# Kernel tuning notes

Hardware: AMD Instinct MI355X
Metric: run time of the kernel (lower is better)

The kernel has to match this reference:

```python
import jax, jax.numpy as jnp
import numpy as np

TOP_K = 8
NUM_EXPERTS = 64
N_TOKENS = 16384
N_EMBED = 4096
EPS = 1e-12  # F.normalize default eps


def setup_inputs() -> dict:
    key = jax.random.key(0)
    k_x, k_wr, k_br, k_wn, k_bn, k_noise = jax.random.split(key, 6)
    scale = 1.0 / np.sqrt(N_EMBED)
    return {
        "x": jax.random.normal(k_x, (N_TOKENS, N_EMBED), dtype=jnp.float32),
        "w_route": jax.random.normal(k_wr, (N_EMBED, NUM_EXPERTS), dtype=jnp.float32) * scale,
        "b_route": jax.random.normal(k_br, (NUM_EXPERTS,), dtype=jnp.float32) * scale,
        "w_noise": jax.random.normal(k_wn, (N_EMBED, NUM_EXPERTS), dtype=jnp.float32) * scale,
        "b_noise": jax.random.normal(k_bn, (NUM_EXPERTS,), dtype=jnp.float32) * scale,
        "noise": jax.random.normal(k_noise, (N_TOKENS, NUM_EXPERTS), dtype=jnp.float32),
    }


def _l1_normalize(v):
    return v / jnp.maximum(jnp.sum(jnp.abs(v)), EPS)


def reference(x, w_route, b_route, w_noise, b_noise, noise):
    # dual linear projections: [N, D] @ [D, E] -> [N, E]
    logits = x @ w_route + b_route
    noise_logits = x @ w_noise + b_noise
    noisy_logits = logits + noise * jax.nn.softplus(noise_logits)

    # top-k (sorted descending, matches torch.topk)
    top_vals, top_idx = jax.lax.top_k(noisy_logits, TOP_K)  # [N, K]
    rows = jnp.arange(noisy_logits.shape[0])[:, None]

    # scatter top-k logits into -inf, softmax -> sparse gate distribution
    sparse_logits = jnp.full_like(noisy_logits, -jnp.inf).at[rows, top_idx].set(top_vals)
    router_output = jax.nn.softmax(sparse_logits, axis=-1)  # [N, E]

    # aux loss (training path). Faithful to torch scatter semantics:
    # gates[n, top_idx[n, j]] = router_output[n, j] (first K columns of src).
    probs = jax.nn.softmax(noisy_logits, axis=-1)
    gates = jnp.zeros_like(probs).at[rows, top_idx].set(router_output[:, :TOP_K])
    probs_sum = probs.sum(0)                                  # [E]
    freq = (gates > 0).astype(jnp.float32).sum(0)             # [E]
    lsesq = jnp.sum(jax.nn.logsumexp(noisy_logits, axis=-1) ** 2)
    switchloss = NUM_EXPERTS * jnp.sum(_l1_normalize(probs_sum) * _l1_normalize(freq))
    zloss = lsesq / noisy_logits.shape[0]
    aux_loss = switchloss + 0.1 * zloss

    return router_output, top_idx, aux_loss
```

## Files before the change

### kernel.cpp

```cpp
#include <hip/hip_runtime.h>
#include <math.h>

#define NT 16384
#define NE 4096
#define NX 64
#define TK 8

#define BM 32
#define NBLK (NT / BM)
#define NSTEP 64

#define RO_SIZE (NT * NX)
#define TI_OFF  RO_SIZE
#define AUX_IDX (RO_SIZE + NT * TK)

#define MAXFLAG 8192
#define PSB_IDX 8256
#define FRB_IDX (PSB_IDX + NBLK * 64)
#define L2B_IDX (FRB_IDX + NBLK * 64)
#define WS_FLOATS (L2B_IDX + NBLK)
#define BPACK_OFF (((WS_FLOATS * 4) + 255) & ~255)
#define BPACK_USHORTS (128 * 4 * 2 * 128 * 8)
#define WS_NEED ((size_t)BPACK_OFF + (size_t)BPACK_USHORTS * 2)

#define DELTA_FP32 5e-5f
#define DELTA_BF16 2.5e-4f

typedef __attribute__((ext_vector_type(8))) short bf16x8_t;
typedef __attribute__((ext_vector_type(4))) float f32x4_t;
typedef __attribute__((ext_vector_type(16))) float f32x16_t;

__device__ __forceinline__ float neginf() { return __int_as_float(0xff800000); }

__device__ __forceinline__ unsigned short bf16_trunc(float f) {
    return (unsigned short)(__float_as_uint(f) >> 16);
}
__device__ __forceinline__ unsigned short bf16_rtn(float f) {
    unsigned u = __float_as_uint(f);
    unsigned r = u + 0x7fffu + ((u >> 16) & 1u);
    return (unsigned short)(r >> 16);
}
__device__ __forceinline__ float bf16_to_f(unsigned short h) {
    return __uint_as_float(((unsigned)h) << 16);
}

__device__ __forceinline__ void split4(const float4& f,
                                       unsigned& h0, unsigned& h1,
                                       unsigned& l0, unsigned& l1) {
    unsigned u0 = __float_as_uint(f.x), u1 = __float_as_uint(f.y);
    unsigned u2 = __float_as_uint(f.z), u3 = __float_as_uint(f.w);
    h0 = __builtin_amdgcn_perm(u1, u0, 0x07060302u);
    h1 = __builtin_amdgcn_perm(u3, u2, 0x07060302u);
    float g0 = f.x - __uint_as_float(u0 & 0xffff0000u);
    float g1 = f.y - __uint_as_float(u1 & 0xffff0000u);
    float g2 = f.z - __uint_as_float(u2 & 0xffff0000u);
    float g3 = f.w - __uint_as_float(u3 & 0xffff0000u);
    l0 = __builtin_amdgcn_perm(__float_as_uint(g1), __float_as_uint(g0), 0x07060302u);
    l1 = __builtin_amdgcn_perm(__float_as_uint(g3), __float_as_uint(g2), 0x07060302u);
}

#define GLOAD16(GP, LP) __builtin_amdgcn_global_load_lds(                     \
    (const __attribute__((address_space(1))) void*)(GP),                      \
    (__attribute__((address_space(3))) void*)(LP), 16, 0, 0)

__global__ __launch_bounds__(512) void prep_w_kernel(
    const float* __restrict__ w_route, const float* __restrict__ w_noise,
    unsigned short* __restrict__ bp)
{
    const int kt = blockIdx.x;
    const int t = threadIdx.x;
    const int col = t & 127;
    const int kq = t >> 7;
    const float* src = (col < NX) ? (w_route + col) : (w_noise + (col - NX));
    const int kbase = kt * 32 + kq * 8;
    bf16x8_t h8, l8;
    #pragma unroll
    for (int i = 0; i < 8; ++i) {
        float v = src[(size_t)(kbase + i) * NX];
        unsigned short hh = bf16_trunc(v);
        h8[i] = (short)hh;
        l8[i] = (short)bf16_rtn(v - bf16_to_f(hh));
    }
    unsigned short* base = bp + ((size_t)((kt * 4 + kq) * 2) * 128 + col) * 8;
    *(bf16x8_t*)base = h8;
    *(bf16x8_t*)(base + 128 * 8) = l8;
}

__global__ __launch_bounds__(512, 4) void fused32_kernel(
    const float* __restrict__ x,
    const unsigned short* __restrict__ bp,
    const float* __restrict__ b_route, const float* __restrict__ b_noise,
    const float* __restrict__ noise,
    float* __restrict__ out,
    float* __restrict__ ps_blk, float* __restrict__ fr_blk,
    float* __restrict__ lse2_blk,
    int* __restrict__ flag_cnt, int* __restrict__ flag_list)
{
    __shared__ __align__(16) char ldsraw[81920];

    const int tid = threadIdx.x;
    const int wid = tid >> 6;
    const int lane = tid & 63;
    const int l31 = lane & 31;
    const int lhi = lane >> 5;
    const int cgq = wid & 3;
    const int kh = wid >> 2;
    const int bm = blockIdx.x * BM;

    const int srow = tid >> 4;
    const int sq = tid & 15;
    const int skc = sq >> 1;
    const int shalf = sq & 1;
    const int srl = srow & 15;
    const int offA = srow * 256 + ((skc ^ srl) << 4) + shalf * 8;
    const float* sxa = x + (size_t)(bm + srow) * NE + sq * 4;

    char* ldsB = ldsraw + 16384;
    char* dB = ldsB + tid * 16;

    #define STAGE_B(BUF, ST) do {                                             \
        const unsigned short* sB_ = bp + (size_t)(ST) * 16384 + tid * 8;      \
        char* dB_ = dB + (BUF) * 32768;                                       \
        GLOAD16(sB_,         dB_);                                            \
        GLOAD16(sB_ + 4096,  dB_ + 8192);                                     \
        GLOAD16(sB_ + 8192,  dB_ + 16384);                                    \
        GLOAD16(sB_ + 12288, dB_ + 24576);                                    \
    } while (0)

    #define WRITE_A(BUF, RX) do {                                             \
        unsigned h0_, h1_, l0_, l1_;                                          \
        split4(RX, h0_, h1_, l0_, l1_);                                       \
        const int ob_ = (BUF) * 8192;                                         \
        *(int2*)(ldsraw + ob_ + offA)         = make_int2((int)h0_, (int)h1_);\
        *(int2*)(ldsraw + ob_ + (offA ^ 128)) = make_int2((int)l0_, (int)l1_);\
    } while (0)

    f32x16_t acc;
    #pragma unroll
    for (int i = 0; i < 16; ++i) acc[i] = 0.f;

    const int r15 = l31 & 15;
    const int adrA0 = l31 * 256 + (((4 * kh + 0 + lhi) ^ r15) << 4);
    const int adrA1 = l31 * 256 + (((4 * kh + 2 + lhi) ^ r15) << 4);
    const int offB = kh * 16384 + lhi * 4096 + (cgq * 32 + l31) * 16;

    #define COMPUTE(CUR) do {                                                 \
        const char* aB_ = ldsraw + (CUR) * 8192;                              \
        const char* bT_ = ldsB + (CUR) * 32768;                               \
        bf16x8_t ah0 = *(const bf16x8_t*)(aB_ + adrA0);                       \
        bf16x8_t al0 = *(const bf16x8_t*)(aB_ + (adrA0 ^ 128));               \
        bf16x8_t bh0 = *(const bf16x8_t*)(bT_ + offB);                        \
        bf16x8_t bl0 = *(const bf16x8_t*)(bT_ + offB + 2048);                 \
        acc = __builtin_amdgcn_mfma_f32_32x32x16_bf16(ah0, bh0, acc, 0, 0, 0);\
        acc = __builtin_amdgcn_mfma_f32_32x32x16_bf16(al0, bh0, acc, 0, 0, 0);\
        acc = __builtin_amdgcn_mfma_f32_32x32x16_bf16(ah0, bl0, acc, 0, 0, 0);\
        bf16x8_t ah1 = *(const bf16x8_t*)(aB_ + adrA1);                       \
        bf16x8_t al1 = *(const bf16x8_t*)(aB_ + (adrA1 ^ 128));               \
        bf16x8_t bh1 = *(const bf16x8_t*)(bT_ + offB + 8192);                 \
        bf16x8_t bl1 = *(const bf16x8_t*)(bT_ + offB + 8192 + 2048);          \
        acc = __builtin_amdgcn_mfma_f32_32x32x16_bf16(ah1, bh1, acc, 0, 0, 0);\
        acc = __builtin_amdgcn_mfma_f32_32x32x16_bf16(al1, bh1, acc, 0, 0, 0);\
        acc = __builtin_amdgcn_mfma_f32_32x32x16_bf16(ah1, bl1, acc, 0, 0, 0);\
    } while (0)

    float4 rxA = *(const float4*)(sxa);
    STAGE_B(0, 0);
    WRITE_A(0, rxA);
    float4 rxB = *(const float4*)(sxa + 64);
    __syncthreads();

    for (int t = 0; t < NSTEP; t += 2) {
        if (t + 2 < NSTEP) rxA = *(const float4*)(sxa + (t + 2) * 64);
        if (t + 1 < NSTEP) STAGE_B(1, t + 1);
        COMPUTE(0);
        if (t + 1 < NSTEP) WRITE_A(1, rxB);
        __syncthreads();
        if (t + 3 < NSTEP) rxB = *(const float4*)(sxa + (t + 3) * 64);
        if (t + 2 < NSTEP) STAGE_B(0, t + 2);
        COMPUTE(1);
        if (t + 2 < NSTEP) WRITE_A(0, rxA);
        __syncthreads();
    }
    #undef STAGE_B
    #undef WRITE_A
    #undef COMPUTE

    float (*part)[32][132] = (float (*)[32][132])ldsraw;
    #pragma unroll
    for (int r = 0; r < 16; ++r) {
        int row = (r & 3) + 8 * (r >> 2) + 4 * lhi;
        part[kh][row][cgq * 32 + l31] = acc[r];
    }
    __syncthreads();

    const float br = b_route[lane];
    const float bnv = b_noise[lane];
    float ps_l = 0.f, fr_l = 0.f, l2_l = 0.f;

    for (int tt = 0; tt < 4; ++tt) {
        const int tok = wid * 4 + tt;
        const int gt  = bm + tok;
        float lr = part[0][tok][lane] + part[1][tok][lane] + br;
        float ln = part[0][tok][64 + lane] + part[1][tok][64 + lane] + bnv;
        float nz = noise[(size_t)gt * NX + lane];
        float sp = fmaxf(ln, 0.f) + log1pf(expf(-fabsf(ln)));
        float v  = lr + nz * sp;

        float vv = v;
        float tv[9]; int ti[9];
        #pragma unroll
        for (int s = 0; s < 9; ++s) {
            float mv = vv; int mi = lane;
            #pragma unroll
            for (int off = 32; off > 0; off >>= 1) {
                float ov = __shfl_xor(mv, off);
                int   oi = __shfl_xor(mi, off);
                if (ov > mv || (ov == mv && oi < mi)) { mv = ov; mi = oi; }
            }
            tv[s] = mv; ti[s] = mi;
            if (lane == mi) vv = neginf();
        }

        float ming = 1e30f;
        #pragma unroll
        for (int s = 0; s < 8; ++s) ming = fminf(ming, tv[s] - tv[s + 1]);
        if (lane == 0 && ming < DELTA_BF16) {
            int p = atomicAdd(flag_cnt, 1);
            if (p < MAXFLAG) flag_list[p] = gt;
        }

        const float m0 = tv[0];
        float e8[8], s8 = 0.f;
        #pragma unroll
        for (int s = 0; s < 8; ++s) { e8[s] = expf(tv[s] - m0); s8 += e8[s]; }
        float r = 0.f;
        #pragma unroll
        for (int s = 0; s < 8; ++s) if (ti[s] == lane) r = e8[s] / s8;
        out[(size_t)gt * NX + lane] = r;
        if (lane < TK) out[TI_OFF + (size_t)gt * TK + lane] = (float)ti[lane];

        float p = expf(v - m0);
        float s64 = p;
        #pragma unroll
        for (int off = 32; off > 0; off >>= 1) s64 += __shfl_xor(s64, off);
        ps_l += p / s64;
        if (lane == 0) { float lse = m0 + logf(s64); l2_l += lse * lse; }

        unsigned tm8 = 0;
        #pragma unroll
        for (int s = 0; s < 8; ++s) if (ti[s] < TK) tm8 |= (1u << ti[s]);
        #pragma unroll
        for (int s = 0; s < 8; ++s)
            if (ti[s] == lane && ((tm8 >> s) & 1u)) fr_l += 1.f;
    }

    float* sps = (float*)(ldsraw + 34816);
    float* sfr = (float*)(ldsraw + 34816 + 2048);
    float* sl2 = (float*)(ldsraw + 34816 + 4096);
    sps[wid * 64 + lane] = ps_l;
    sfr[wid * 64 + lane] = fr_l;
    if (lane == 0) sl2[wid] = l2_l;
    __syncthreads();
    if (wid == 0) {
        float a = 0.f, b = 0.f;
        #pragma unroll
        for (int w = 0; w < 8; ++w) {
            a += sps[w * 64 + lane];
            b += sfr[w * 64 + lane];
        }
        ps_blk[(size_t)blockIdx.x * 64 + lane] = a;
        fr_blk[(size_t)blockIdx.x * 64 + lane] = b;
        if (lane == 0) {
            float z = 0.f;
            #pragma unroll
            for (int w = 0; w < 8; ++w) z += sl2[w];
            lse2_blk[blockIdx.x] = z;
        }
    }
}

#define FBM 64
#define FBN 128
#define FBK 32
#define XPITCH (FBM + 4)
__global__ __launch_bounds__(256) void fused_router_kernel(
    const float* __restrict__ x,
    const float* __restrict__ w_route, const float* __restrict__ b_route,
    const float* __restrict__ w_noise, const float* __restrict__ b_noise,
    const float* __restrict__ noise,
    float* __restrict__ out,
    float* __restrict__ ps_acc, float* __restrict__ fr_acc,
    float* __restrict__ lse2_acc,
    int* __restrict__ flag_cnt, int* __restrict__ flag_list)
{
    __shared__ float smem[FBM * FBN];
    float* xs  = smem;
    float* wst = smem + FBK * XPITCH;
    const int tid = threadIdx.x;
    const int block_m = blockIdx.x * FBM;
    const int row0 = (tid >> 5) * 8;
    const int col0 = (tid & 31) * 4;
    float acc[8][4];
    #pragma unroll
    for (int i = 0; i < 8; ++i)
        #pragma unroll
        for (int j = 0; j < 4; ++j) acc[i][j] = 0.f;
    float4 px[2], pw[4];
    {
        #pragma unroll
        for (int s = 0; s < 2; ++s) {
            int f = tid + s * 256, r = f >> 3, kqv = f & 7;
            px[s] = *reinterpret_cast<const float4*>(x + (size_t)(block_m + r) * NE + kqv * 4);
        }
        #pragma unroll
        for (int s = 0; s < 4; ++s) {
            int f = tid + s * 256, kk = f >> 5, c4 = (f & 31) * 4;
            const float* src = (c4 < NX) ? (w_route + (size_t)kk * NX + c4)
                                         : (w_noise + (size_t)kk * NX + (c4 - NX));
            pw[s] = *reinterpret_cast<const float4*>(src);
        }
    }
    for (int t = 0; t < NE / FBK; ++t) {
        __syncthreads();
        #pragma unroll
        for (int s = 0; s < 2; ++s) {
            int f = tid + s * 256, r = f >> 3, kqv = f & 7;
            xs[(kqv * 4 + 0) * XPITCH + r] = px[s].x;
            xs[(kqv * 4 + 1) * XPITCH + r] = px[s].y;
            xs[(kqv * 4 + 2) * XPITCH + r] = px[s].z;
            xs[(kqv * 4 + 3) * XPITCH + r] = px[s].w;
        }
        #pragma unroll
        for (int s = 0; s < 4; ++s) {
            int f = tid + s * 256, kk = f >> 5, c4 = (f & 31) * 4;
            *reinterpret_cast<float4*>(&wst[kk * FBN + c4]) = pw[s];
        }
        __syncthreads();
        if (t + 1 < NE / FBK) {
            const int k0 = (t + 1) * FBK;
            #pragma unroll
            for (int s = 0; s < 2; ++s) {
                int f = tid + s * 256, r = f >> 3, kqv = f & 7;
                px[s] = *reinterpret_cast<const float4*>(x + (size_t)(block_m + r) * NE + k0 + kqv * 4);
            }
            #pragma unroll
            for (int s = 0; s < 4; ++s) {
                int f = tid + s * 256, kk = f >> 5, c4 = (f & 31) * 4;
                const float* src = (c4 < NX) ? (w_route + (size_t)(k0 + kk) * NX + c4)
                                             : (w_noise + (size_t)(k0 + kk) * NX + (c4 - NX));
                pw[s] = *reinterpret_cast<const float4*>(src);
            }
        }
        #pragma unroll
        for (int k = 0; k < FBK; ++k) {
            float4 xa = *reinterpret_cast<const float4*>(&xs[k * XPITCH + row0]);
            float4 xb = *reinterpret_cast<const float4*>(&xs[k * XPITCH + row0 + 4]);
            float4 wv = *reinterpret_cast<const float4*>(&wst[k * FBN + col0]);
            float xf[8] = {xa.x, xa.y, xa.z, xa.w, xb.x, xb.y, xb.z, xb.w};
            float wf[4] = {wv.x, wv.y, wv.z, wv.w};
            #pragma unroll
            for (int i = 0; i < 8; ++i)
                #pragma unroll
                for (int j = 0; j < 4; ++j)
                    acc[i][j] = fmaf(xf[i], wf[j], acc[i][j]);
        }
    }
    __syncthreads();
    #pragma unroll
    for (int i = 0; i < 8; ++i) {
        float4 v = make_float4(acc[i][0], acc[i][1], acc[i][2], acc[i][3]);
        *reinterpret_cast<float4*>(&smem[(row0 + i) * FBN + col0]) = v;
    }
    __syncthreads();
    const int wave = tid >> 6;
    const int lane = tid & 63;
    const float br = b_route[lane];
    const float bnv = b_noise[lane];
    float ps_l = 0.f, fr_l = 0.f, l2_l = 0.f;
    for (int tt = 0; tt < FBM / 4; ++tt) {
        const int tok = wave * (FBM / 4) + tt;
        const int gt  = block_m + tok;
        float lr = smem[tok * FBN + lane] + br;
        float ln = smem[tok * FBN + NX + lane] + bnv;
        float nz = noise[(size_t)gt * NX + lane];
        float sp = fmaxf(ln, 0.f) + log1pf(expf(-fabsf(ln)));
        float v  = lr + nz * sp;
        float vv = v;
        float tv[9]; int ti[9];
        #pragma unroll
        for (int s = 0; s < 9; ++s) {
            float mv = vv; int mi = lane;
            #pragma unroll
            for (int off = 32; off > 0; off >>= 1) {
                float ov = __shfl_xor(mv, off);
                int   oi = __shfl_xor(mi, off);
                if (ov > mv || (ov == mv && oi < mi)) { mv = ov; mi = oi; }
            }
            tv[s] = mv; ti[s] = mi;
            if (lane == mi) vv = neginf();
        }
        float ming = 1e30f;
        #pragma unroll
        for (int s = 0; s < 8; ++s) ming = fminf(ming, tv[s] - tv[s + 1]);
        if (lane == 0 && ming < DELTA_FP32) {
            int p = atomicAdd(flag_cnt, 1);
            if (p < MAXFLAG) flag_list[p] = gt;
        }
        const float m0 = tv[0];
        float e8[8], s8 = 0.f;
        #pragma unroll
        for (int s = 0; s < 8; ++s) { e8[s] = expf(tv[s] - m0); s8 += e8[s]; }
        float r = 0.f;
        #pragma unroll
        for (int s = 0; s < 8; ++s) if (ti[s] == lane) r = e8[s] / s8;
        out[(size_t)gt * NX + lane] = r;
        if (lane < TK) out[TI_OFF + (size_t)gt * TK + lane] = (float)ti[lane];
        float p = expf(v - m0);
        float s64 = p;
        #pragma unroll
        for (int off = 32; off > 0; off >>= 1) s64 += __shfl_xor(s64, off);
        ps_l += p / s64;
        if (lane == 0) { float lse = m0 + logf(s64); l2_l += lse * lse; }
        unsigned tm8 = 0;
        #pragma unroll
        for (int s = 0; s < 8; ++s) if (ti[s] < TK) tm8 |= (1u << ti[s]);
        #pragma unroll
        for (int s = 0; s < 8; ++s)
            if (ti[s] == lane && ((tm8 >> s) & 1u)) fr_l += 1.f;
    }
    atomicAdd(&ps_acc[lane], ps_l);
    atomicAdd(&fr_acc[lane], fr_l);
    if (lane == 0) atomicAdd(lse2_acc, l2_l);
}

__global__ __launch_bounds__(256) void refine_kernel(
    const float* __restrict__ x, const float* __restrict__ w_route,
    const float* __restrict__ b_route, const float* __restrict__ w_noise,
    const float* __restrict__ b_noise, const float* __restrict__ noise,
    float* __restrict__ out, const int* __restrict__ flag_cnt,
    const int* __restrict__ flag_list)
{
    __shared__ double red[8][64];
    const int tid = threadIdx.x;
    const int lane = tid & 63, wq = tid >> 6;
    int nf = *flag_cnt; if (nf > MAXFLAG) nf = MAXFLAG;
    for (int fi = blockIdx.x; fi < nf; fi += gridDim.x) {
        const int gt = flag_list[fi];
        const float* xr = x + (size_t)gt * NE + wq * 1024;
        const float* wr = w_route + (size_t)wq * 1024 * NX;
        const float* wn = w_noise + (size_t)wq * 1024 * NX;
        double ar0 = 0, ar1 = 0, an0 = 0, an1 = 0;
        for (int k = 0; k < 1024; k += 2) {
            double x0 = xr[k], x1 = xr[k + 1];
            ar0 += x0 * (double)wr[(size_t)k * NX + lane];
            ar1 += x1 * (double)wr[(size_t)(k + 1) * NX + lane];
            an0 += x0 * (double)wn[(size_t)k * NX + lane];
            an1 += x1 * (double)wn[(size_t)(k + 1) * NX + lane];
        }
        red[wq * 2][lane]     = ar0 + ar1;
        red[wq * 2 + 1][lane] = an0 + an1;
        __syncthreads();
        if (tid < 64) {
            double lr = red[0][lane] + red[2][lane] + red[4][lane] + red[6][lane]
                      + (double)b_route[lane];
            double ln = red[1][lane] + red[3][lane] + red[5][lane] + red[7][lane]
                      + (double)b_noise[lane];
            double nz = (double)noise[(size_t)gt * NX + lane];
            double sp = (ln > 0.0) ? (ln + log1p(exp(-ln))) : log1p(exp(ln));
            double v  = lr + nz * sp;
            double vv = v;
            double tv[8]; int ti[8];
            #pragma unroll
            for (int s = 0; s < 8; ++s) {
                double mv = vv; int mi = lane;
                #pragma unroll
                for (int off = 32; off > 0; off >>= 1) {
                    double ov = __shfl_xor(mv, off);
                    int    oi = __shfl_xor(mi, off);
                    if (ov > mv || (ov == mv && oi < mi)) { mv = ov; mi = oi; }
                }
                tv[s] = mv; ti[s] = mi;
                if (lane == mi) vv = -1.0e300;
            }
            double m0 = tv[0], s8 = 0.0, e8[8];
            #pragma unroll
            for (int s = 0; s < 8; ++s) { e8[s] = exp(tv[s] - m0); s8 += e8[s]; }
            float r = 0.f;
            #pragma unroll
            for (int s = 0; s < 8; ++s) if (ti[s] == lane) r = (float)(e8[s] / s8);
            out[(size_t)gt * NX + lane] = r;
            if (lane < TK) out[TI_OFF + (size_t)gt * TK + lane] = (float)ti[lane];
        }
        __syncthreads();
    }
}

__global__ __launch_bounds__(512) void finalize_kernel(
    const float* __restrict__ ps_blk, const float* __restrict__ fr_blk,
    const float* __restrict__ lse2_blk, float* __restrict__ out)
{
    __shared__ float sps[8][64], sfr[8][64], sl2[512];
    const int t = threadIdx.x;
    const int e = t & 63, g = t >> 6;
    float a = 0.f, b = 0.f;
    for (int blk = g; blk < NBLK; blk += 8) {
        a += ps_blk[(size_t)blk * 64 + e];
        b += fr_blk[(size_t)blk * 64 + e];
    }
    sps[g][e] = a;
    sfr[g][e] = b;
    sl2[t] = lse2_blk[t];
    __syncthreads();
    if (t < 64) {
        float p = 0.f, f = 0.f;
        #pragma unroll
        for (int gg = 0; gg < 8; ++gg) { p += sps[gg][t]; f += sfr[gg][t]; }
        float z = 0.f;
        #pragma unroll
        for (int i = 0; i < 8; ++i) z += sl2[t * 8 + i];
        float sp = p, sf = f, sz = z;
        #pragma unroll
        for (int off = 32; off > 0; off >>= 1) {
            sp += __shfl_xor(sp, off);
            sf += __shfl_xor(sf, off);
            sz += __shfl_xor(sz, off);
        }
        float d = (p / fmaxf(sp, 1e-12f)) * (f / fmaxf(sf, 1e-12f));
        #pragma unroll
        for (int off = 32; off > 0; off >>= 1) d += __shfl_xor(d, off);
        if (t == 0)
            out[AUX_IDX] = 64.f * d + 0.1f * (sz / (float)NT);
    }
}

extern "C" void kernel_launch(void* const* d_in, const int* in_sizes, int n_in,
                              void* d_out, int out_size, void* d_ws, size_t ws_size,
                              hipStream_t stream) {
    const float* x       = (const float*)d_in[0];
    const float* w_route = (const float*)d_in[1];
    const float* b_route = (const float*)d_in[2];
    const float* w_noise = (const float*)d_in[3];
    const float* b_noise = (const float*)d_in[4];
    const float* noise   = (const float*)d_in[5];
    float* out = (float*)d_out;

    float* wsf = (float*)d_ws;
    int* flag_cnt  = (int*)wsf;
    int* flag_list = (int*)(wsf + 1);
    float* ps_blk   = wsf + PSB_IDX;
    float* fr_blk   = wsf + FRB_IDX;
    float* lse2_blk = wsf + L2B_IDX;

    hipMemsetAsync(d_ws, 0, (size_t)(1 + MAXFLAG) * sizeof(int), stream);

    if (ws_size >= WS_NEED) {
        unsigned short* bpack = (unsigned short*)((char*)d_ws + BPACK_OFF);
        prep_w_kernel<<<128, 512, 0, stream>>>(w_route, w_noise, bpack);
        fused32_kernel<<<NBLK, 512, 0, stream>>>(
            x, bpack, b_route, b_noise, noise, out,
            ps_blk, fr_blk, lse2_blk, flag_cnt, flag_list);
    } else {
        hipMemsetAsync(ps_blk, 0,
                       (size_t)(WS_FLOATS - PSB_IDX) * sizeof(float), stream);
        fused_router_kernel<<<NT / FBM, 256, 0, stream>>>(
            x, w_route, b_route, w_noise, b_noise, noise, out,
            ps_blk, fr_blk, lse2_blk, flag_cnt, flag_list);
    }

    refine_kernel<<<1024, 256, 0, stream>>>(
        x, w_route, b_route, w_noise, b_noise, noise, out, flag_cnt, flag_list);

    finalize_kernel<<<1, 512, 0, stream>>>(ps_blk, fr_blk, lse2_blk, out);
}
```

Baseline: 193.8 us.

## Split K four ways across waves, each wave computing two column tiles

Remaps the eight waves so that each covers a quarter of the K slice per step and computes two 32-column output tiles, instead of half of K for one tile. Each A fragment loaded from LDS now feeds two MFMA chains, which halves A reads per MFMA and gives two independent accumulator chains to hide MFMA latency. The cost is a second accumulator (more VGPRs), a four-way partial-sum reduction in LDS, and moving the reduction scratch to a higher LDS offset. A change to the fallback kernel's w_route pointer computes the same address as before.

```diff
diff --git a/kernel.cpp b/kernel.cpp
--- a/kernel.cpp
+++ b/kernel.cpp
@@ -103,8 +103,8 @@
     const int lane = tid & 63;
     const int l31 = lane & 31;
     const int lhi = lane >> 5;
-    const int cgq = wid & 3;
-    const int kh = wid >> 2;
+    const int cgp = wid & 1;
+    const int kh = wid >> 1;
     const int bm = blockIdx.x * BM;
 
     const int srow = tid >> 4;
@@ -135,32 +135,31 @@
         *(int2*)(ldsraw + ob_ + (offA ^ 128)) = make_int2((int)l0_, (int)l1_);\
     } while (0)
 
-    f32x16_t acc;
+    f32x16_t acc0, acc1;
     #pragma unroll
-    for (int i = 0; i < 16; ++i) acc[i] = 0.f;
+    for (int i = 0; i < 16; ++i) { acc0[i] = 0.f; acc1[i] = 0.f; }
 
     const int r15 = l31 & 15;
-    const int adrA0 = l31 * 256 + (((4 * kh + 0 + lhi) ^ r15) << 4);
-    const int adrA1 = l31 * 256 + (((4 * kh + 2 + lhi) ^ r15) << 4);
-    const int offB = kh * 16384 + lhi * 4096 + (cgq * 32 + l31) * 16;
+    const int adrA = l31 * 256 + (((2 * kh + lhi) ^ r15) << 4);
+    const int offB0 = (kh >> 1) * 16384 + ((kh & 1) * 2 + lhi) * 4096
+                    + (cgp * 64 + l31) * 16;
+    const int offB1 = offB0 + 512;
 
     #define COMPUTE(CUR) do {                                                 \
         const char* aB_ = ldsraw + (CUR) * 8192;                              \
         const char* bT_ = ldsB + (CUR) * 32768;                               \
-        bf16x8_t ah0 = *(const bf16x8_t*)(aB_ + adrA0);                       \
-        bf16x8_t al0 = *(const bf16x8_t*)(aB_ + (adrA0 ^ 128));               \
-        bf16x8_t bh0 = *(const bf16x8_t*)(bT_ + offB);                        \
-        bf16x8_t bl0 = *(const bf16x8_t*)(bT_ + offB + 2048);                 \
-        acc = __builtin_amdgcn_mfma_f32_32x32x16_bf16(ah0, bh0, acc, 0, 0, 0);\
-        acc = __builtin_amdgcn_mfma_f32_32x32x16_bf16(al0, bh0, acc, 0, 0, 0);\
-        acc = __builtin_amdgcn_mfma_f32_32x32x16_bf16(ah0, bl0, acc, 0, 0, 0);\
-        bf16x8_t ah1 = *(const bf16x8_t*)(aB_ + adrA1);                       \
-        bf16x8_t al1 = *(const bf16x8_t*)(aB_ + (adrA1 ^ 128));               \
-        bf16x8_t bh1 = *(const bf16x8_t*)(bT_ + offB + 8192);                 \
-        bf16x8_t bl1 = *(const bf16x8_t*)(bT_ + offB + 8192 + 2048);          \
-        acc = __builtin_amdgcn_mfma_f32_32x32x16_bf16(ah1, bh1, acc, 0, 0, 0);\
-        acc = __builtin_amdgcn_mfma_f32_32x32x16_bf16(al1, bh1, acc, 0, 0, 0);\
-        acc = __builtin_amdgcn_mfma_f32_32x32x16_bf16(ah1, bl1, acc, 0, 0, 0);\
+        bf16x8_t ah  = *(const bf16x8_t*)(aB_ + adrA);                        \
+        bf16x8_t al  = *(const bf16x8_t*)(aB_ + (adrA ^ 128));                \
+        bf16x8_t bh0 = *(const bf16x8_t*)(bT_ + offB0);                       \
+        bf16x8_t bh1 = *(const bf16x8_t*)(bT_ + offB1);                       \
+        bf16x8_t bl0 = *(const bf16x8_t*)(bT_ + offB0 + 2048);                \
+        bf16x8_t bl1 = *(const bf16x8_t*)(bT_ + offB1 + 2048);                \
+        acc0 = __builtin_amdgcn_mfma_f32_32x32x16_bf16(ah, bh0, acc0, 0, 0, 0);\
+        acc1 = __builtin_amdgcn_mfma_f32_32x32x16_bf16(ah, bh1, acc1, 0, 0, 0);\
+        acc0 = __builtin_amdgcn_mfma_f32_32x32x16_bf16(al, bh0, acc0, 0, 0, 0);\
+        acc1 = __builtin_amdgcn_mfma_f32_32x32x16_bf16(al, bh1, acc1, 0, 0, 0);\
+        acc0 = __builtin_amdgcn_mfma_f32_32x32x16_bf16(ah, bl0, acc0, 0, 0, 0);\
+        acc1 = __builtin_amdgcn_mfma_f32_32x32x16_bf16(ah, bl1, acc1, 0, 0, 0);\
     } while (0)
 
     float4 rxA = *(const float4*)(sxa);
@@ -189,7 +188,8 @@
     #pragma unroll
     for (int r = 0; r < 16; ++r) {
         int row = (r & 3) + 8 * (r >> 2) + 4 * lhi;
-        part[kh][row][cgq * 32 + l31] = acc[r];
+        part[kh][row][cgp * 64 + l31]      = acc0[r];
+        part[kh][row][cgp * 64 + 32 + l31] = acc1[r];
     }
     __syncthreads();
 
@@ -200,8 +200,10 @@
     for (int tt = 0; tt < 4; ++tt) {
         const int tok = wid * 4 + tt;
         const int gt  = bm + tok;
-        float lr = part[0][tok][lane] + part[1][tok][lane] + br;
-        float ln = part[0][tok][64 + lane] + part[1][tok][64 + lane] + bnv;
+        float lr = part[0][tok][lane] + part[1][tok][lane]
+                 + part[2][tok][lane] + part[3][tok][lane] + br;
+        float ln = part[0][tok][64 + lane] + part[1][tok][64 + lane]
+                 + part[2][tok][64 + lane] + part[3][tok][64 + lane] + bnv;
         float nz = noise[(size_t)gt * NX + lane];
         float sp = fmaxf(ln, 0.f) + log1pf(expf(-fabsf(ln)));
         float v  = lr + nz * sp;
@@ -254,9 +256,9 @@
             if (ti[s] == lane && ((tm8 >> s) & 1u)) fr_l += 1.f;
     }
 
-    float* sps = (float*)(ldsraw + 34816);
-    float* sfr = (float*)(ldsraw + 34816 + 2048);
-    float* sl2 = (float*)(ldsraw + 34816 + 4096);
+    float* sps = (float*)(ldsraw + 69632);
+    float* sfr = (float*)(ldsraw + 69632 + 2048);
+    float* sl2 = (float*)(ldsraw + 69632 + 4096);
     sps[wid * 64 + lane] = ps_l;
     sfr[wid * 64 + lane] = fr_l;
     if (lane == 0) sl2[wid] = l2_l;
@@ -346,8 +348,9 @@
             #pragma unroll
             for (int s = 0; s < 4; ++s) {
                 int f = tid + s * 256, kk = f >> 5, c4 = (f & 31) * 4;
-                const float* src = (c4 < NX) ? (w_route + (size_t)(k0 + kk) * NX + c4)
+                const float* src = (c4 < NX) ? (w_route + (size_t)kk * NX + c4)
                                              : (w_noise + (size_t)(k0 + kk) * NX + (c4 - NX));
+                if (c4 < NX) src = w_route + (size_t)(k0 + kk) * NX + c4;
                 pw[s] = *reinterpret_cast<const float4*>(src);
             }
         }
```

After: 199.9 us. 3.1% more time.

## Double block to 1024 threads with four-way K split in fused router kernel

Applied to the files above, without the earlier changes.

Launches the fused 32-token kernel with 1024 threads, so 16 waves split the K dimension four ways instead of two. Each wave now issues three MFMAs per stage instead of six, and each thread stages half as much of the packed weight tile. Only the first 512 threads load and split the x tile. The epilogue sums four partial accumulators and each wave handles two tokens instead of four. The aim is more in-flight waves to hide memory latency, at the cost of a larger LDS partial-sum region, extra reduction adds, and barriers over more waves.

```diff
diff --git a/kernel.cpp b/kernel.cpp
--- a/kernel.cpp
+++ b/kernel.cpp
@@ -86,7 +86,7 @@
     *(bf16x8_t*)(base + 128 * 8) = l8;
 }
 
-__global__ __launch_bounds__(512, 4) void fused32_kernel(
+__global__ __launch_bounds__(1024, 8) void fused32_kernel(
     const float* __restrict__ x,
     const unsigned short* __restrict__ bp,
     const float* __restrict__ b_route, const float* __restrict__ b_noise,
@@ -106,8 +106,9 @@
     const int cgq = wid & 3;
     const int kh = wid >> 2;
     const int bm = blockIdx.x * BM;
-
-    const int srow = tid >> 4;
+    const bool stager = (tid < 512);
+
+    const int srow = (tid >> 4) & 31;
     const int sq = tid & 15;
     const int skc = sq >> 1;
     const int shalf = sq & 1;
@@ -122,17 +123,17 @@
         const unsigned short* sB_ = bp + (size_t)(ST) * 16384 + tid * 8;      \
         char* dB_ = dB + (BUF) * 32768;                                       \
         GLOAD16(sB_,         dB_);                                            \
-        GLOAD16(sB_ + 4096,  dB_ + 8192);                                     \
         GLOAD16(sB_ + 8192,  dB_ + 16384);                                    \
-        GLOAD16(sB_ + 12288, dB_ + 24576);                                    \
     } while (0)
 
     #define WRITE_A(BUF, RX) do {                                             \
-        unsigned h0_, h1_, l0_, l1_;                                          \
-        split4(RX, h0_, h1_, l0_, l1_);                                       \
-        const int ob_ = (BUF) * 8192;                                         \
-        *(int2*)(ldsraw + ob_ + offA)         = make_int2((int)h0_, (int)h1_);\
-        *(int2*)(ldsraw + ob_ + (offA ^ 128)) = make_int2((int)l0_, (int)l1_);\
+        if (stager) {                                                         \
+            unsigned h0_, h1_, l0_, l1_;                                      \
+            split4(RX, h0_, h1_, l0_, l1_);                                   \
+            const int ob_ = (BUF) * 8192;                                     \
+            *(int2*)(ldsraw + ob_ + offA)         = make_int2((int)h0_, (int)h1_);\
+            *(int2*)(ldsraw + ob_ + (offA ^ 128)) = make_int2((int)l0_, (int)l1_);\
+        }                                                                     \
     } while (0)
 
     f32x16_t acc;
@@ -140,42 +141,36 @@
     for (int i = 0; i < 16; ++i) acc[i] = 0.f;
 
     const int r15 = l31 & 15;
-    const int adrA0 = l31 * 256 + (((4 * kh + 0 + lhi) ^ r15) << 4);
-    const int adrA1 = l31 * 256 + (((4 * kh + 2 + lhi) ^ r15) << 4);
-    const int offB = kh * 16384 + lhi * 4096 + (cgq * 32 + l31) * 16;
+    const int adrA = l31 * 256 + (((2 * kh + lhi) ^ r15) << 4);
+    const int offB = (kh >> 1) * 16384 + ((kh & 1) * 2 + lhi) * 4096
+                   + (cgq * 32 + l31) * 16;
 
     #define COMPUTE(CUR) do {                                                 \
         const char* aB_ = ldsraw + (CUR) * 8192;                              \
         const char* bT_ = ldsB + (CUR) * 32768;                               \
-        bf16x8_t ah0 = *(const bf16x8_t*)(aB_ + adrA0);                       \
-        bf16x8_t al0 = *(const bf16x8_t*)(aB_ + (adrA0 ^ 128));               \
-        bf16x8_t bh0 = *(const bf16x8_t*)(bT_ + offB);                        \
-        bf16x8_t bl0 = *(const bf16x8_t*)(bT_ + offB + 2048);                 \
-        acc = __builtin_amdgcn_mfma_f32_32x32x16_bf16(ah0, bh0, acc, 0, 0, 0);\
-        acc = __builtin_amdgcn_mfma_f32_32x32x16_bf16(al0, bh0, acc, 0, 0, 0);\
-        acc = __builtin_amdgcn_mfma_f32_32x32x16_bf16(ah0, bl0, acc, 0, 0, 0);\
-        bf16x8_t ah1 = *(const bf16x8_t*)(aB_ + adrA1);                       \
-        bf16x8_t al1 = *(const bf16x8_t*)(aB_ + (adrA1 ^ 128));               \
-        bf16x8_t bh1 = *(const bf16x8_t*)(bT_ + offB + 8192);                 \
-        bf16x8_t bl1 = *(const bf16x8_t*)(bT_ + offB + 8192 + 2048);          \
-        acc = __builtin_amdgcn_mfma_f32_32x32x16_bf16(ah1, bh1, acc, 0, 0, 0);\
-        acc = __builtin_amdgcn_mfma_f32_32x32x16_bf16(al1, bh1, acc, 0, 0, 0);\
-        acc = __builtin_amdgcn_mfma_f32_32x32x16_bf16(ah1, bl1, acc, 0, 0, 0);\
+        bf16x8_t ah = *(const bf16x8_t*)(aB_ + adrA);                         \
+        bf16x8_t al = *(const bf16x8_t*)(aB_ + (adrA ^ 128));                 \
+        bf16x8_t bh = *(const bf16x8_t*)(bT_ + offB);                         \
+        bf16x8_t bl = *(const bf16x8_t*)(bT_ + offB + 2048);                  \
+        acc = __builtin_amdgcn_mfma_f32_32x32x16_bf16(ah, bh, acc, 0, 0, 0);  \
+        acc = __builtin_amdgcn_mfma_f32_32x32x16_bf16(al, bh, acc, 0, 0, 0);  \
+        acc = __builtin_amdgcn_mfma_f32_32x32x16_bf16(ah, bl, acc, 0, 0, 0);  \
     } while (0)
 
-    float4 rxA = *(const float4*)(sxa);
+    float4 rxA, rxB;
+    if (stager) rxA = *(const float4*)(sxa);
     STAGE_B(0, 0);
     WRITE_A(0, rxA);
-    float4 rxB = *(const float4*)(sxa + 64);
+    if (stager) rxB = *(const float4*)(sxa + 64);
     __syncthreads();
 
     for (int t = 0; t < NSTEP; t += 2) {
-        if (t + 2 < NSTEP) rxA = *(const float4*)(sxa + (t + 2) * 64);
+        if (stager && t + 2 < NSTEP) rxA = *(const float4*)(sxa + (t + 2) * 64);
         if (t + 1 < NSTEP) STAGE_B(1, t + 1);
         COMPUTE(0);
         if (t + 1 < NSTEP) WRITE_A(1, rxB);
         __syncthreads();
-        if (t + 3 < NSTEP) rxB = *(const float4*)(sxa + (t + 3) * 64);
+        if (stager && t + 3 < NSTEP) rxB = *(const float4*)(sxa + (t + 3) * 64);
         if (t + 2 < NSTEP) STAGE_B(0, t + 2);
         COMPUTE(1);
         if (t + 2 < NSTEP) WRITE_A(0, rxA);
@@ -197,11 +192,13 @@
     const float bnv = b_noise[lane];
     float ps_l = 0.f, fr_l = 0.f, l2_l = 0.f;
 
-    for (int tt = 0; tt < 4; ++tt) {
-        const int tok = wid * 4 + tt;
+    for (int tt = 0; tt < 2; ++tt) {
+        const int tok = wid * 2 + tt;
         const int gt  = bm + tok;
-        float lr = part[0][tok][lane] + part[1][tok][lane] + br;
-        float ln = part[0][tok][64 + lane] + part[1][tok][64 + lane] + bnv;
+        float lr = part[0][tok][lane] + part[1][tok][lane]
+                 + part[2][tok][lane] + part[3][tok][lane] + br;
+        float ln = part[0][tok][64 + lane] + part[1][tok][64 + lane]
+                 + part[2][tok][64 + lane] + part[3][tok][64 + lane] + bnv;
         float nz = noise[(size_t)gt * NX + lane];
         float sp = fmaxf(ln, 0.f) + log1pf(expf(-fabsf(ln)));
         float v  = lr + nz * sp;
@@ -254,9 +251,9 @@
             if (ti[s] == lane && ((tm8 >> s) & 1u)) fr_l += 1.f;
     }
 
-    float* sps = (float*)(ldsraw + 34816);
-    float* sfr = (float*)(ldsraw + 34816 + 2048);
-    float* sl2 = (float*)(ldsraw + 34816 + 4096);
+    float* sps = (float*)(ldsraw + 69632);
+    float* sfr = (float*)(ldsraw + 69632 + 4096);
+    float* sl2 = (float*)(ldsraw + 69632 + 8192);
     sps[wid * 64 + lane] = ps_l;
     sfr[wid * 64 + lane] = fr_l;
     if (lane == 0) sl2[wid] = l2_l;
@@ -264,7 +261,7 @@
     if (wid == 0) {
         float a = 0.f, b = 0.f;
         #pragma unroll
-        for (int w = 0; w < 8; ++w) {
+        for (int w = 0; w < 16; ++w) {
             a += sps[w * 64 + lane];
             b += sfr[w * 64 + lane];
         }
@@ -273,7 +270,7 @@
         if (lane == 0) {
             float z = 0.f;
             #pragma unroll
-            for (int w = 0; w < 8; ++w) z += sl2[w];
+            for (int w = 0; w < 16; ++w) z += sl2[w];
             lse2_blk[blockIdx.x] = z;
         }
     }
@@ -556,7 +553,7 @@
     if (ws_size >= WS_NEED) {
         unsigned short* bpack = (unsigned short*)((char*)d_ws + BPACK_OFF);
         prep_w_kernel<<<128, 512, 0, stream>>>(w_route, w_noise, bpack);
-        fused32_kernel<<<NBLK, 512, 0, stream>>>(
+        fused32_kernel<<<NBLK, 1024, 0, stream>>>(
             x, bpack, b_route, b_noise, noise, out,
             ps_blk, fr_blk, lse2_blk, flag_cnt, flag_list);
     } else {
```

Measured after the change: 193.1 us. No clear change (-0.4%).
